# Kernel tuning notes

Measured on AMD Instinct MI355X. Metric: run time of the kernel, lower is better.

The kernel has to match this reference:

```python
import jax, jax.numpy as jnp
import numpy as np

COMMITMENT_COST = 0.25
DECAY = 0.99
EPSILON = 1e-05
NUM_EMBEDDINGS = 1024
EMBEDDING_DIM = 256


def setup_inputs() -> dict:
    key = jax.random.key(0)
    k1, k2, k3 = jax.random.split(key, 3)
    B, T, D, K = 32, 1024, EMBEDDING_DIM, NUM_EMBEDDINGS
    z = jax.random.normal(k1, (B, T, D), dtype=jnp.float32)
    # torch init is uniform(-1/K, 1/K); scaled normal is fine for a numeric reference
    embedding = jax.random.uniform(k2, (K, D), dtype=jnp.float32, minval=-1.0 / K, maxval=1.0 / K)
    ema_cluster_size = jnp.ones((K,), dtype=jnp.float32)
    ema_w = embedding.copy()
    return {"z": z, "embedding": embedding, "ema_cluster_size": ema_cluster_size, "ema_w": ema_w}


def reference(z, embedding, ema_cluster_size, ema_w):
    B, T, D = z.shape
    K = embedding.shape[0]
    flat_z = z.reshape(-1, D)                         # [N, D]
    # squared L2 distances: ||z||^2 + ||e||^2 - 2 z.e   -> [N, K]
    distances = (jnp.sum(flat_z * flat_z, axis=1, keepdims=True)
                 + jnp.sum(embedding * embedding, axis=1)
                 - 2.0 * flat_z @ embedding.T)
    encoding_indices = jnp.argmin(distances, axis=1)  # [N]
    quantized = embedding[encoding_indices].reshape(B, T, D)

    # EMA codebook update (training branch; buffers, no grad)
    cluster_counts = jax.ops.segment_sum(jnp.ones_like(encoding_indices, dtype=jnp.float32),
                                         encoding_indices, num_segments=K)
    new_cluster_size = ema_cluster_size * DECAY + (1.0 - DECAY) * cluster_counts
    n = jnp.sum(new_cluster_size)
    new_cluster_size = (new_cluster_size + EPSILON) / (n + K * EPSILON) * n
    dw = jax.ops.segment_sum(flat_z, encoding_indices, num_segments=K)  # [K, D]
    new_ema_w = ema_w * DECAY + (1.0 - DECAY) * dw
    new_embedding = new_ema_w / new_cluster_size[:, None]

    commitment_loss = jnp.mean((z - jax.lax.stop_gradient(quantized)) ** 2)
    loss = COMMITMENT_COST * commitment_loss
    # straight-through estimator
    quantized_st = z + jax.lax.stop_gradient(quantized - z)
    return (quantized_st, loss, encoding_indices.reshape(B, T),
            new_cluster_size, new_ema_w, new_embedding)
```

## Files before the change

### kernel.cpp

```cpp
#include <hip/hip_runtime.h>
#include <hip/hip_fp16.h>
#include <math.h>

#define COMMITMENT_COST 0.25f
#define DECAY 0.99f
#define EPSILON 1e-05f
#define KCODES 1024
#define DIM 256
#define NTOK 32768

#define O_QUANT 0
#define O_LOSS  8388608
#define O_IDX   8388609
#define O_CS    8421377
#define O_EMAW  8422401
#define O_EMB   8684545

#define SE_IDX    0
#define SE_ESQ    32768
#define SE_ZSQ    33792
#define SE_HIST   66560
#define SE_NM     67584
#define SE_NOVF   67585
#define SE_MLIST  67586
#define SE_OVF    100354
#define SE_OFFS   133122
#define SE_CUR    134147
#define SE_TLIST  135171
#define SE_LPART  167939

#define SQ_ZH    0
#define SQ_EH    4194304
#define SQ_MG    4325376
#define SQ_CC    4358144
#define SQ_CAND  4390912

#define THETA_F 2e-3f
#define CAND_CAP 16
#define EPSC 2e-4f

typedef __attribute__((ext_vector_type(8))) _Float16 f16x8;
typedef __attribute__((ext_vector_type(4))) float f32x4;

__global__ void pre_kernel(const float* __restrict__ z, const float* __restrict__ E,
                           float* __restrict__ zsq, float* __restrict__ esq,
                           int* __restrict__ hist, float* __restrict__ loss,
                           unsigned short* __restrict__ zh,
                           unsigned short* __restrict__ eh,
                           int* __restrict__ nm, int* __restrict__ novf) {
    const int b = blockIdx.x;
    const int wave = threadIdx.x >> 6;
    const int lane = threadIdx.x & 63;
    if (b < NTOK / 4) {
        int token = b * 4 + wave;
        float4 v = ((const float4*)(z + (size_t)token * DIM))[lane];
        ushort4 h;
        h.x = __half_as_ushort(__float2half(v.x));
        h.y = __half_as_ushort(__float2half(v.y));
        h.z = __half_as_ushort(__float2half(v.z));
        h.w = __half_as_ushort(__float2half(v.w));
        *(ushort4*)(zh + (size_t)token * DIM + lane * 4) = h;
        float s = v.x * v.x + v.y * v.y + v.z * v.z + v.w * v.w;
        #pragma unroll
        for (int off = 32; off > 0; off >>= 1) s += __shfl_down(s, off);
        if (lane == 0) zsq[token] = s;
        if (b == 0 && threadIdx.x == 4) loss[0] = 0.0f;
        if (b == 0 && threadIdx.x == 5) { *nm = 0; *novf = 0; }
    } else {
        int eb = b - NTOK / 4;
        int k = eb * 4 + wave;
        float4 v = ((const float4*)(E + (size_t)k * DIM))[lane];
        ushort4 h;
        h.x = __half_as_ushort(__float2half(v.x));
        h.y = __half_as_ushort(__float2half(v.y));
        h.z = __half_as_ushort(__float2half(v.z));
        h.w = __half_as_ushort(__float2half(v.w));
        *(ushort4*)(eh + (size_t)k * DIM + lane * 4) = h;
        float s = v.x * v.x + v.y * v.y + v.z * v.z + v.w * v.w;
        #pragma unroll
        for (int off = 32; off > 0; off >>= 1) s += __shfl_down(s, off);
        if (lane == 0) esq[k] = s;
        if (threadIdx.x < 4) hist[eb * 4 + threadIdx.x] = 0;
    }
}

__global__ __launch_bounds__(256) void dist_mfma_kernel(
        const unsigned short* __restrict__ zh, const unsigned short* __restrict__ eh,
        const float* __restrict__ esq,
        float* __restrict__ Mg, int* __restrict__ ccount,
        unsigned long long* __restrict__ cand) {
    __shared__ unsigned short Als[64 * 264];
    __shared__ unsigned short Bls[128 * 40];
    __shared__ float scr[64][4];
    __shared__ float runmin[64];
    __shared__ int lcnt[64];

    const int tid = threadIdx.x;
    const int wn = tid >> 6;
    const int lane = tid & 63;
    const int l15 = lane & 15, l4 = lane >> 4;
    const int tok0 = blockIdx.x * 64;

    #pragma unroll
    for (int q = 0; q < 8; ++q) {
        int c = tid + 256 * q;
        int row = c >> 5, ch = c & 31;
        *(f16x8*)(Als + row * 264 + ch * 8) =
            *(const f16x8*)(zh + (size_t)(tok0 + row) * 256 + ch * 8);
    }
    if (tid < 64) { runmin[tid] = 3.4e38f; lcnt[tid] = 0; }
    __syncthreads();

    const int brow0 = tid >> 2, bch = tid & 3;

    for (int c0 = 0; c0 < KCODES; c0 += 128) {
        f32x4 acc[4][2];
        #pragma unroll
        for (int i = 0; i < 4; ++i)
            #pragma unroll
            for (int j = 0; j < 2; ++j)
                acc[i][j] = (f32x4){0.f, 0.f, 0.f, 0.f};

        for (int kt = 0; kt < 8; ++kt) {
            const int kk = kt * 32;
            f16x8 b0 = *(const f16x8*)(
                eh + (size_t)(c0 + brow0) * 256 + kk + bch * 8);
            f16x8 b1 = *(const f16x8*)(
                eh + (size_t)(c0 + brow0 + 64) * 256 + kk + bch * 8);
            __syncthreads();
            *(f16x8*)(Bls + brow0 * 40 + bch * 8) = b0;
            *(f16x8*)(Bls + (brow0 + 64) * 40 + bch * 8) = b1;
            __syncthreads();
            f16x8 av[4], bv[2];
            #pragma unroll
            for (int i = 0; i < 4; ++i)
                av[i] = *(const f16x8*)(Als + (i * 16 + l15) * 264 + kk + l4 * 8);
            #pragma unroll
            for (int j = 0; j < 2; ++j)
                bv[j] = *(const f16x8*)(Bls + (wn * 32 + j * 16 + l15) * 40 + l4 * 8);
            #pragma unroll
            for (int i = 0; i < 4; ++i)
                #pragma unroll
                for (int j = 0; j < 2; ++j)
                    acc[i][j] = __builtin_amdgcn_mfma_f32_16x16x32_f16(
                        av[i], bv[j], acc[i][j], 0, 0, 0);
        }

        float sq[2];
        #pragma unroll
        for (int j = 0; j < 2; ++j) sq[j] = esq[c0 + wn * 32 + j * 16 + l15];

        #pragma unroll
        for (int i = 0; i < 4; ++i) {
            #pragma unroll
            for (int r = 0; r < 4; ++r) {
                float v = fminf(sq[0] - 2.0f * acc[i][0][r],
                                sq[1] - 2.0f * acc[i][1][r]);
                #pragma unroll
                for (int m = 1; m < 16; m <<= 1)
                    v = fminf(v, __shfl_xor(v, m));
                if (l15 == 0) scr[i * 16 + l4 * 4 + r][wn] = v;
            }
        }
        __syncthreads();
        if (tid < 64) {
            float m = fminf(fminf(scr[tid][0], scr[tid][1]),
                            fminf(scr[tid][2], scr[tid][3]));
            runmin[tid] = fminf(runmin[tid], m);
        }
        __syncthreads();
        #pragma unroll
        for (int i = 0; i < 4; ++i) {
            #pragma unroll
            for (int r = 0; r < 4; ++r) {
                const int row = i * 16 + l4 * 4 + r;
                const float thr = runmin[row] + THETA_F;
                #pragma unroll
                for (int j = 0; j < 2; ++j) {
                    float d = sq[j] - 2.0f * acc[i][j][r];
                    if (d <= thr) {
                        int slot = atomicAdd(&lcnt[row], 1);
                        if (slot < CAND_CAP)
                            cand[(size_t)slot * NTOK + tok0 + row] =
                                (((unsigned long long)__float_as_uint(d)) << 32) |
                                (unsigned)(c0 + wn * 32 + j * 16 + l15);
                    }
                }
            }
        }
    }
    __syncthreads();
    if (tid < 64) {
        Mg[tok0 + tid] = runmin[tid];
        ccount[tok0 + tid] = lcnt[tid];
    }
}

__global__ __launch_bounds__(256) void recheck_a_kernel(
        const float* __restrict__ Mg, const int* __restrict__ ccount,
        const unsigned long long* __restrict__ cand,
        unsigned int* __restrict__ idx,
        int* __restrict__ mlist, int* __restrict__ nm,
        int* __restrict__ ovf, int* __restrict__ novf) {
    __shared__ int ps[256];
    __shared__ int base_m, base_o;
    const int tid = threadIdx.x;
    const int token = blockIdx.x * 256 + tid;
    const int cnt = ccount[token];
    const float thr = Mg[token] + THETA_F;

    const bool isovf_cap = (cnt > CAND_CAP);
    int nsurv = 0;
    int firstcode = 0;
    if (!isovf_cap) {
        for (int s = 0; s < cnt; ++s) {
            unsigned long long e = cand[(size_t)s * NTOK + token];
            float dt = __uint_as_float((unsigned)(e >> 32));
            if (dt <= thr) {
                ++nsurv;
                if (nsurv == 1) firstcode = (int)(unsigned)(e & 0x3FFull);
            }
        }
    }
    const bool ismulti = !isovf_cap && nsurv >= 2 && nsurv <= 8;
    const bool isovf = isovf_cap || (!isovf_cap && (nsurv == 0 || nsurv > 8));
    const int want = (ismulti ? 1 : 0) | ((isovf ? 1 : 0) << 16);

    ps[tid] = want;
    __syncthreads();
    #pragma unroll
    for (int off = 1; off < 256; off <<= 1) {
        int v = (tid >= off) ? ps[tid - off] : 0;
        __syncthreads();
        ps[tid] += v;
        __syncthreads();
    }
    if (tid == 255) {
        int tot = ps[255];
        base_m = (tot & 0xFFFF) ? atomicAdd(nm, tot & 0xFFFF) : 0;
        base_o = (tot >> 16) ? atomicAdd(novf, tot >> 16) : 0;
    }
    __syncthreads();
    const int off_m = (ps[tid] - want) & 0xFFFF;
    const int off_o = (ps[tid] - want) >> 16;

    if (!isovf_cap && nsurv == 1) idx[token] = (unsigned)firstcode;
    if (ismulti) mlist[base_m + off_m] = token;
    if (isovf)   ovf[base_o + off_o] = token;
}

#define RB_BLOCKS 1024
__global__ __launch_bounds__(256) void recheck_b_kernel(
        const float* __restrict__ z, const float* __restrict__ E,
        const float* __restrict__ zsq, const float* __restrict__ esq,
        const float* __restrict__ Mg, const int* __restrict__ ccount,
        const unsigned long long* __restrict__ cand,
        const int* __restrict__ mlist, const int* __restrict__ nm,
        const int* __restrict__ ovf, const int* __restrict__ novf,
        unsigned int* __restrict__ idx) {
    const int wave = threadIdx.x >> 6, lane = threadIdx.x & 63;
    const int gw = blockIdx.x * 4 + wave;
    const int n = *nm;
    for (int m = gw; m < n; m += RB_BLOCKS * 4) {
        const int token = mlist[m];
        const int cnt = ccount[token];
        const float thr = Mg[token] + THETA_F;
        const float An = zsq[token];
        const float4 zv = *(const float4*)(z + (size_t)token * DIM + lane * 4);
        unsigned long long e = 0x7F80000000000000ull;
        if (lane < cnt) e = cand[(size_t)lane * NTOK + token];
        const float dt = __uint_as_float((unsigned)(e >> 32));
        const int ec = (int)(unsigned)(e & 0x3FFull);
        const unsigned long long bm0 = __ballot(lane < cnt && dt <= thr);
        unsigned long long bm = bm0;
        const int ns = __popcll(bm0);

        float m1 = 3.4e38f, m2 = 3.4e38f; int a1 = 0x7fffffff;
        int mycode = 0; float mydv = 3.4e38f;
        #pragma unroll
        for (int i = 0; i < 8; ++i) {
            if (i < ns) {
                const int s = __ffsll(bm) - 1; bm &= bm - 1;
                const int code = __shfl(ec, s);
                const float4 ev = *(const float4*)(E + (size_t)code * DIM + lane * 4);
                float p = fmaf(zv.x, ev.x, 0.0f);
                p = fmaf(zv.y, ev.y, p);
                p = fmaf(zv.z, ev.z, p);
                p = fmaf(zv.w, ev.w, p);
                #pragma unroll
                for (int o = 1; o < 64; o <<= 1) p += __shfl_xor(p, o);
                const float dv = (An + esq[code]) - 2.0f * p;
                if (dv < m1 || (dv == m1 && code < a1)) { m2 = m1; m1 = dv; a1 = code; }
                else if (dv < m2) m2 = dv;
                if (lane == i) { mycode = code; mydv = dv; }
            }
        }
        if (m2 - m1 > 2.0f * EPSC) {
            if (lane == 0) idx[token] = (unsigned)a1;
        } else {
            float b1 = 3.4e38f; int ai = 0x7fffffff;
            for (int s = 0; s < ns; ++s) {
                const int code = __shfl(mycode, s);
                const float dvp = __shfl(mydv, s);
                if (dvp <= m1 + 2.0f * EPSC && lane == 0) {
                    const float4* zp = (const float4*)(z + (size_t)token * DIM);
                    const float4* ep = (const float4*)(E + (size_t)code * DIM);
                    float acc = 0.0f;
                    #pragma unroll 8
                    for (int q = 0; q < 64; ++q) {
                        float4 a = zp[q], b = ep[q];
                        acc = fmaf(a.x, b.x, acc); acc = fmaf(a.y, b.y, acc);
                        acc = fmaf(a.z, b.z, acc); acc = fmaf(a.w, b.w, acc);
                    }
                    float dv = (An + esq[code]) - 2.0f * acc;
                    if (dv < b1 || (dv == b1 && code < ai)) { b1 = dv; ai = code; }
                }
            }
            if (lane == 0) idx[token] = (unsigned)ai;
        }
    }
    const int nov = *novf;
    for (int w = gw; w < nov; w += RB_BLOCKS * 4) {
        const int token = ovf[w];
        const float An = zsq[token];
        const float4* zp = (const float4*)(z + (size_t)token * DIM);
        float best = 3.4e38f; int bid = 0x7fffffff;
        for (int code = lane; code < KCODES; code += 64) {
            const float4* ep = (const float4*)(E + (size_t)code * DIM);
            float acc = 0.0f;
            for (int q = 0; q < 64; ++q) {
                float4 a = zp[q], b = ep[q];
                acc = fmaf(a.x, b.x, acc); acc = fmaf(a.y, b.y, acc);
                acc = fmaf(a.z, b.z, acc); acc = fmaf(a.w, b.w, acc);
            }
            float dv = (An + esq[code]) - 2.0f * acc;
            if (dv < best || (dv == best && code < bid)) { best = dv; bid = code; }
        }
        #pragma unroll
        for (int mm = 1; mm < 64; mm <<= 1) {
            float ov = __shfl_xor(best, mm); int oi = __shfl_xor(bid, mm);
            if (ov < best || (ov == best && oi < bid)) { best = ov; bid = oi; }
        }
        if (lane == 0) idx[token] = (unsigned)bid;
    }
}

__global__ __launch_bounds__(256) void mid_kernel(
        const float* __restrict__ z, const float* __restrict__ E,
        const unsigned int* __restrict__ idxarr,
        float* __restrict__ idx_out, int* __restrict__ hist,
        float* __restrict__ quant, float* __restrict__ lpart) {
    __shared__ float ls[4];
    const int wave = threadIdx.x >> 6;
    const int lane = threadIdx.x & 63;
    const int token = blockIdx.x * 4 + wave;
    const int idx = (int)idxarr[token];

    if (lane == 0) {
        idx_out[token] = (float)idx;
        atomicAdd(&hist[idx], 1);
    }

    const float4 ev = *(const float4*)(E + (size_t)idx * DIM + lane * 4);
    const float4 zv = *(const float4*)(z + (size_t)token * DIM + lane * 4);
    *(float4*)(quant + (size_t)token * DIM + lane * 4) = ev;

    float dx = zv.x - ev.x, dy = zv.y - ev.y, dz = zv.z - ev.z, dww = zv.w - ev.w;
    float l = dx * dx + dy * dy + dz * dz + dww * dww;
    #pragma unroll
    for (int off = 32; off > 0; off >>= 1) l += __shfl_down(l, off);
    if (lane == 0) ls[wave] = l;
    __syncthreads();
    if (threadIdx.x == 0)
        lpart[blockIdx.x] = (ls[0] + ls[1]) + (ls[2] + ls[3]);
}

__global__ __launch_bounds__(256) void cs_kernel(
        const int* __restrict__ hist, const float* __restrict__ ema_cs,
        float* __restrict__ cs_out, int* __restrict__ offs,
        int* __restrict__ cursor, const float* __restrict__ lpart,
        float* __restrict__ loss) {
    __shared__ float f[256];
    __shared__ int hs[256];
    const int tid = threadIdx.x;
    float pre4[4]; int h4[4];
    float part = 0.0f; int hp = 0;
    #pragma unroll
    for (int q = 0; q < 4; ++q) {
        int k = tid * 4 + q;
        h4[q] = hist[k];
        pre4[q] = ema_cs[k] * DECAY + (1.0f - DECAY) * (float)h4[q];
        part += pre4[q];
        hp += h4[q];
    }
    f[tid] = part; hs[tid] = hp;
    __syncthreads();
    #pragma unroll
    for (int off = 1; off < 256; off <<= 1) {
        int v = (tid >= off) ? hs[tid - off] : 0;
        __syncthreads();
        hs[tid] += v;
        __syncthreads();
    }
    int run = hs[tid] - hp;
    #pragma unroll
    for (int q = 0; q < 4; ++q) {
        int k = tid * 4 + q;
        offs[k] = run; cursor[k] = run;
        run += h4[q];
    }
    if (tid == 255) offs[KCODES] = run;
    for (int s = 128; s > 0; s >>= 1) {
        if (tid < s) f[tid] += f[tid + s];
        __syncthreads();
    }
    float n = f[0];
    #pragma unroll
    for (int q = 0; q < 4; ++q) {
        int k = tid * 4 + q;
        cs_out[k] = (pre4[q] + EPSILON) / (n + KCODES * EPSILON) * n;
    }
    float lp = 0.0f;
    #pragma unroll
    for (int q = 0; q < 32; ++q) lp += lpart[tid + 256 * q];
    __syncthreads();
    f[tid] = lp;
    __syncthreads();
    for (int s = 128; s > 0; s >>= 1) {
        if (tid < s) f[tid] += f[tid + s];
        __syncthreads();
    }
    if (tid == 0) loss[0] = f[0];
}

__global__ __launch_bounds__(256) void scatter_kernel(
        const unsigned int* __restrict__ idxarr,
        int* __restrict__ cursor, int* __restrict__ tlist) {
    const int t = blockIdx.x * 256 + threadIdx.x;
    const int idx = (int)idxarr[t];
    const int pos = atomicAdd(&cursor[idx], 1);
    tlist[pos] = t;
}

__global__ __launch_bounds__(256) void fin_gather_kernel(
        const float* __restrict__ z, const int* __restrict__ offs,
        const int* __restrict__ tlist, float* __restrict__ dw) {
    __shared__ float4 red[4][64];
    const int k = blockIdx.x;
    const int grp = threadIdx.x >> 6;
    const int lane = threadIdx.x & 63;
    const int s = offs[k], e = offs[k + 1];
    float4 acc = {0.f, 0.f, 0.f, 0.f};
    for (int i = s + grp; i < e; i += 4) {
        const int t = tlist[i];
        const float4 v = *(const float4*)(z + (size_t)t * DIM + lane * 4);
        acc.x += v.x; acc.y += v.y; acc.z += v.z; acc.w += v.w;
    }
    red[grp][lane] = acc;
    __syncthreads();
    if (grp == 0) {
        float4 a = red[0][lane], b = red[1][lane];
        float4 c = red[2][lane], d = red[3][lane];
        float4 o;
        o.x = (a.x + b.x) + (c.x + d.x);
        o.y = (a.y + b.y) + (c.y + d.y);
        o.z = (a.z + b.z) + (c.z + d.z);
        o.w = (a.w + b.w) + (c.w + d.w);
        *(float4*)(dw + (size_t)k * DIM + lane * 4) = o;
    }
}

__global__ __launch_bounds__(256) void fin_kernel(
        const float* __restrict__ ema_w, const float* __restrict__ cs,
        float* __restrict__ emaw_inout , float* __restrict__ emb_out,
        float* __restrict__ loss_inout) {
    const int i = blockIdx.x * 256 + threadIdx.x;
    const int k = i >> 6;
    float4 d = ((const float4*)emaw_inout)[i];
    float4 w = ((const float4*)ema_w)[i];
    float4 nw;
    nw.x = w.x * DECAY + (1.0f - DECAY) * d.x;
    nw.y = w.y * DECAY + (1.0f - DECAY) * d.y;
    nw.z = w.z * DECAY + (1.0f - DECAY) * d.z;
    nw.w = w.w * DECAY + (1.0f - DECAY) * d.w;
    ((float4*)emaw_inout)[i] = nw;
    float inv = 1.0f / cs[k];
    float4 e; e.x = nw.x * inv; e.y = nw.y * inv; e.z = nw.z * inv; e.w = nw.w * inv;
    ((float4*)emb_out)[i] = e;
    if (i == 0)
        loss_inout[0] = COMMITMENT_COST * loss_inout[0] / (float)((size_t)NTOK * DIM);
}

extern "C" void kernel_launch(void* const* d_in, const int* in_sizes, int n_in,
                              void* d_out, int out_size, void* d_ws, size_t ws_size,
                              hipStream_t stream) {
    const float* z      = (const float*)d_in[0];
    const float* E      = (const float*)d_in[1];
    const float* ema_cs = (const float*)d_in[2];
    const float* ema_w  = (const float*)d_in[3];
    float* out = (float*)d_out;

    float* emb = out + O_EMB;
    unsigned int* idx = (unsigned int*)(emb + SE_IDX);
    float* esq  = emb + SE_ESQ;
    float* zsq  = emb + SE_ZSQ;
    int*   hist = (int*)(emb + SE_HIST);
    int*   nm     = (int*)(emb + SE_NM);
    int*   novf   = (int*)(emb + SE_NOVF);
    int*   mlist  = (int*)(emb + SE_MLIST);
    int*   ovf    = (int*)(emb + SE_OVF);
    int*   offs   = (int*)(emb + SE_OFFS);
    int*   cursor = (int*)(emb + SE_CUR);
    int*   tlist  = (int*)(emb + SE_TLIST);
    float* lpart  = emb + SE_LPART;

    unsigned short* zh = (unsigned short*)(out + SQ_ZH);
    unsigned short* eh = (unsigned short*)(out + SQ_EH);
    float* Mg = out + SQ_MG;
    int* ccount = (int*)(out + SQ_CC);
    unsigned long long* cand = (unsigned long long*)(out + SQ_CAND);

    pre_kernel<<<NTOK / 4 + KCODES / 4, 256, 0, stream>>>(
        z, E, zsq, esq, hist, out + O_LOSS, zh, eh, nm, novf);
    dist_mfma_kernel<<<NTOK / 64, 256, 0, stream>>>(
        zh, eh, esq, Mg, ccount, cand);
    recheck_a_kernel<<<NTOK / 256, 256, 0, stream>>>(
        Mg, ccount, cand, idx, mlist, nm, ovf, novf);
    recheck_b_kernel<<<RB_BLOCKS, 256, 0, stream>>>(
        z, E, zsq, esq, Mg, ccount, cand, mlist, nm, ovf, novf, idx);
    mid_kernel<<<NTOK / 4, 256, 0, stream>>>(z, E, idx, out + O_IDX, hist,
                                             out + O_QUANT, lpart);
    cs_kernel<<<1, 256, 0, stream>>>(hist, ema_cs, out + O_CS, offs, cursor,
                                     lpart, out + O_LOSS);
    scatter_kernel<<<NTOK / 256, 256, 0, stream>>>(idx, cursor, tlist);
    fin_gather_kernel<<<KCODES, 256, 0, stream>>>(z, offs, tlist, out + O_EMAW);
    fin_kernel<<<256, 256, 0, stream>>>(ema_w, out + O_CS, out + O_EMAW, emb,
                                        out + O_LOSS);
}
```

Baseline: 239.5 us.

## Double-buffer codebook tiles and widen code tile to 256 in distance kernel

The MFMA distance kernel now processes 256 codes per outer iteration instead of 128, so each wave holds a 4x4 accumulator block. The B (codebook) shared tile is double-buffered: the next k-slice is loaded into registers before the MFMAs and written to the other buffer afterward, leaving one barrier per k-step instead of two. LDS row padding also changes (264->260, 40->36), which alters the bank-conflict pattern. The cost is more registers and LDS, which may reduce occupancy.

```diff
diff --git a/kernel.cpp b/kernel.cpp
--- a/kernel.cpp
+++ b/kernel.cpp
@@ -89,8 +89,8 @@
         const float* __restrict__ esq,
         float* __restrict__ Mg, int* __restrict__ ccount,
         unsigned long long* __restrict__ cand) {
-    __shared__ unsigned short Als[64 * 264];
-    __shared__ unsigned short Bls[128 * 40];
+    __shared__ unsigned short Als[64 * 260];
+    __shared__ unsigned short Bls[2][256 * 36];
     __shared__ float scr[64][4];
     __shared__ float runmin[64];
     __shared__ int lcnt[64];
@@ -105,57 +105,74 @@
     for (int q = 0; q < 8; ++q) {
         int c = tid + 256 * q;
         int row = c >> 5, ch = c & 31;
-        *(f16x8*)(Als + row * 264 + ch * 8) =
+        *(f16x8*)(Als + row * 260 + ch * 8) =
             *(const f16x8*)(zh + (size_t)(tok0 + row) * 256 + ch * 8);
     }
     if (tid < 64) { runmin[tid] = 3.4e38f; lcnt[tid] = 0; }
-    __syncthreads();
-
-    const int brow0 = tid >> 2, bch = tid & 3;
-
-    for (int c0 = 0; c0 < KCODES; c0 += 128) {
-        f32x4 acc[4][2];
+
+    const int brow = tid >> 2, bch = tid & 3;
+
+    #pragma unroll
+    for (int q = 0; q < 4; ++q) {
+        f16x8 r = *(const f16x8*)(eh + (size_t)(brow + 64 * q) * 256 + bch * 8);
+        *(f16x8*)(Bls[0] + (brow + 64 * q) * 36 + bch * 8) = r;
+    }
+    __syncthreads();
+
+    int cur = 0;
+    for (int c0 = 0; c0 < KCODES; c0 += 256) {
+        f32x4 acc[4][4];
         #pragma unroll
         for (int i = 0; i < 4; ++i)
             #pragma unroll
-            for (int j = 0; j < 2; ++j)
+            for (int j = 0; j < 4; ++j)
                 acc[i][j] = (f32x4){0.f, 0.f, 0.f, 0.f};
 
         for (int kt = 0; kt < 8; ++kt) {
-            const int kk = kt * 32;
-            f16x8 b0 = *(const f16x8*)(
-                eh + (size_t)(c0 + brow0) * 256 + kk + bch * 8);
-            f16x8 b1 = *(const f16x8*)(
-                eh + (size_t)(c0 + brow0 + 64) * 256 + kk + bch * 8);
-            __syncthreads();
-            *(f16x8*)(Bls + brow0 * 40 + bch * 8) = b0;
-            *(f16x8*)(Bls + (brow0 + 64) * 40 + bch * 8) = b1;
-            __syncthreads();
-            f16x8 av[4], bv[2];
+            int nc0 = c0, nkt = kt + 1;
+            if (nkt == 8) { nkt = 0; nc0 += 256; }
+            const bool hasnext = (nc0 < KCODES);
+            f16x8 rn[4];
+            if (hasnext) {
+                #pragma unroll
+                for (int q = 0; q < 4; ++q)
+                    rn[q] = *(const f16x8*)(
+                        eh + (size_t)(nc0 + brow + 64 * q) * 256 + nkt * 32 + bch * 8);
+            }
+            f16x8 av[4], bv[4];
             #pragma unroll
             for (int i = 0; i < 4; ++i)
-                av[i] = *(const f16x8*)(Als + (i * 16 + l15) * 264 + kk + l4 * 8);
+                av[i] = *(const f16x8*)(Als + (i * 16 + l15) * 260 + kt * 32 + l4 * 8);
             #pragma unroll
-            for (int j = 0; j < 2; ++j)
-                bv[j] = *(const f16x8*)(Bls + (wn * 32 + j * 16 + l15) * 40 + l4 * 8);
+            for (int j = 0; j < 4; ++j)
+                bv[j] = *(const f16x8*)(Bls[cur] + (wn * 64 + j * 16 + l15) * 36 + l4 * 8);
             #pragma unroll
             for (int i = 0; i < 4; ++i)
                 #pragma unroll
-                for (int j = 0; j < 2; ++j)
+                for (int j = 0; j < 4; ++j)
                     acc[i][j] = __builtin_amdgcn_mfma_f32_16x16x32_f16(
                         av[i], bv[j], acc[i][j], 0, 0, 0);
-        }
-
-        float sq[2];
-        #pragma unroll
-        for (int j = 0; j < 2; ++j) sq[j] = esq[c0 + wn * 32 + j * 16 + l15];
+            if (hasnext) {
+                #pragma unroll
+                for (int q = 0; q < 4; ++q)
+                    *(f16x8*)(Bls[cur ^ 1] + (brow + 64 * q) * 36 + bch * 8) = rn[q];
+            }
+            __syncthreads();
+            cur ^= 1;
+        }
+
+        float sq[4];
+        #pragma unroll
+        for (int j = 0; j < 4; ++j) sq[j] = esq[c0 + wn * 64 + j * 16 + l15];
 
         #pragma unroll
         for (int i = 0; i < 4; ++i) {
             #pragma unroll
             for (int r = 0; r < 4; ++r) {
-                float v = fminf(sq[0] - 2.0f * acc[i][0][r],
-                                sq[1] - 2.0f * acc[i][1][r]);
+                float v = fminf(fminf(sq[0] - 2.0f * acc[i][0][r],
+                                      sq[1] - 2.0f * acc[i][1][r]),
+                                fminf(sq[2] - 2.0f * acc[i][2][r],
+                                      sq[3] - 2.0f * acc[i][3][r]));
                 #pragma unroll
                 for (int m = 1; m < 16; m <<= 1)
                     v = fminf(v, __shfl_xor(v, m));
@@ -176,14 +193,14 @@
                 const int row = i * 16 + l4 * 4 + r;
                 const float thr = runmin[row] + THETA_F;
                 #pragma unroll
-                for (int j = 0; j < 2; ++j) {
+                for (int j = 0; j < 4; ++j) {
                     float d = sq[j] - 2.0f * acc[i][j][r];
                     if (d <= thr) {
                         int slot = atomicAdd(&lcnt[row], 1);
                         if (slot < CAND_CAP)
                             cand[(size_t)slot * NTOK + tok0 + row] =
                                 (((unsigned long long)__float_as_uint(d)) << 32) |
-                                (unsigned)(c0 + wn * 32 + j * 16 + l15);
+                                (unsigned)(c0 + wn * 64 + j * 16 + l15);
                     }
                 }
             }
```

Measured after the change: 223.6 us. -6.7%, faster.
